# Kernel tuning notes

Hardware: AMD Instinct MI355X
Metric: run time of the kernel (lower is better)

The kernel has to match this reference:

```python
import jax, jax.numpy as jnp
import numpy as np

B = 16384
INPUT_DIM = 2048
HIDDEN = 1536
N_COMP = 256
N_LAYERS = 32
TOP_K = 4


def setup_inputs() -> dict:
    key = jax.random.key(0)
    ks = jax.random.split(key, 12)
    s_in = 1.0 / np.sqrt(INPUT_DIM)
    s_h = 1.0 / np.sqrt(HIDDEN)
    s_3 = 1.0 / np.sqrt(3)
    return {
        "x": jax.random.normal(ks[0], (B, INPUT_DIM), dtype=jnp.float32),
        "layer_idx": 3,
        "embed": jax.random.normal(ks[1], (N_LAYERS, INPUT_DIM), dtype=jnp.float32),
        "enc_w1": jax.random.uniform(ks[2], (INPUT_DIM, HIDDEN), jnp.float32, -s_in, s_in),
        "enc_b1": jax.random.uniform(ks[3], (HIDDEN,), jnp.float32, -s_in, s_in),
        "enc_w2": jax.random.uniform(ks[4], (HIDDEN, N_COMP), jnp.float32, -s_h, s_h),
        "enc_b2": jax.random.uniform(ks[5], (N_COMP,), jnp.float32, -s_h, s_h),
        "components": jax.random.normal(ks[6], (N_COMP, 3), dtype=jnp.float32),
        "dec_w1": jax.random.uniform(ks[7], (3, HIDDEN), jnp.float32, -s_3, s_3),
        "dec_b1": jax.random.uniform(ks[8], (HIDDEN,), jnp.float32, -s_3, s_3),
        "dec_w2": jax.random.uniform(ks[9], (HIDDEN, INPUT_DIM), jnp.float32, -s_h, s_h),
        "dec_b2": jax.random.uniform(ks[10], (INPUT_DIM,), jnp.float32, -s_h, s_h),
    }


def reference(x, layer_idx, embed, enc_w1, enc_b1, enc_w2, enc_b2,
              components, dec_w1, dec_b1, dec_w2, dec_b2):
    # x: (B, D). Add per-layer embedding row.
    x = x + embed[layer_idx]
    # Encoder MLP: Linear -> GELU (exact, erf-based like torch default) -> Linear
    h = jax.nn.gelu(x @ enc_w1 + enc_b1, approximate=False)
    logits = h @ enc_w2 + enc_b2                     # (B, C)
    # Top-k gated masked softmax: softmax over only the top_k logits per row.
    vals, idx = jax.lax.top_k(logits, TOP_K)         # (B, K), (B, K)
    w = jax.nn.softmax(vals, axis=-1)                # (B, K)
    # Sparse mix: equivalent to masked_fill(-inf) softmax @ components
    pts = jnp.einsum('bk,bkc->bc', w, components[idx])  # (B, 3)
    # Decoder MLP
    d = jax.nn.gelu(pts @ dec_w1 + dec_b1, approximate=False)
    decoded = d @ dec_w2 + dec_b2                    # (B, D)
    encoded = jnp.broadcast_to(components[None], (x.shape[0], N_COMP, 3))
    return encoded, decoded
```

## Files before the change

### kernel.cpp

```cpp
#include <hip/hip_runtime.h>


typedef float  f32x4  __attribute__((ext_vector_type(4)));
typedef short  short8 __attribute__((ext_vector_type(8)));
typedef int    i32x4  __attribute__((ext_vector_type(4)));

#define DEVINL __device__ __forceinline__

constexpr int  NB      = 16384;
constexpr int  IN_DIM  = 2048;
constexpr int  HID     = 1536;
constexpr int  NC      = 256;
constexpr long ENC_ELEMS = (long)NB * NC * 3;
constexpr float TAU  = 2e-5f;
constexpr float TAU1 = 1.5e-3f;
constexpr int  MAXR  = 64;
constexpr int  M2CAP = 2048;
constexpr int  NKT1 = IN_DIM / 32;
constexpr int  NKT2 = HID / 32;

constexpr float SCALE_X  = 3251.2f;
constexpr float SCALE_W1 = 1471325.0f;
constexpr float SCALE_H  = 4644.5714f;
constexpr float SCALE_W2 = 1274205.0f;
constexpr double INV_S1 = 1.0 / ((double)SCALE_X * (double)SCALE_W1);
constexpr double INV_S2 = 1.0 / ((double)SCALE_H * (double)SCALE_W2);
constexpr float C_DA     = 3.0f;
constexpr float SCALE_DA = 39.08f;
constexpr float SCALE_W2D = 4977.0f;
constexpr double INV_SD = 1.0 / ((double)SCALE_DA * (double)SCALE_W2D);

DEVINL unsigned short f2bf(float f) {
  unsigned int u = __builtin_bit_cast(unsigned int, f);
  u = u + 0x7fffu + ((u >> 16) & 1u);
  return (unsigned short)(u >> 16);
}
DEVINL float bf2f(unsigned short h) {
  unsigned int u = ((unsigned int)h) << 16;
  return __builtin_bit_cast(float, u);
}
DEVINL float gelu_f(float v) {
  return 0.5f * v * (1.0f + erff(v * 0.70710678118654752440f));
}
DEVINL void llds16(const void* g, void* l) {
  __builtin_amdgcn_global_load_lds(
      (const __attribute__((address_space(1))) void*)g,
      (__attribute__((address_space(3))) void*)l, 16, 0, 0);
}
DEVINL f32x4 mfma_bf16(short8 a, short8 b, f32x4 c) {
  return __builtin_amdgcn_mfma_f32_16x16x32_bf16(a, b, c, 0, 0, 0);
}
DEVINL i32x4 mfma_i8(i32x4 a, i32x4 b, i32x4 c) {
  return __builtin_amdgcn_mfma_i32_16x16x64_i8(a, b, c, 0, 0, 0);
}
DEVINL long packed_off(long tileIdx, int rowp, int kq, int e) {
  int slot = kq ^ ((rowp >> 1) & 3);
  return (tileIdx * 512 + rowp * 4 + slot) * 8 + e;
}
DEVINL int swz_idx(int rowp, int kq) {
  return (rowp * 4 + (kq ^ ((rowp >> 1) & 3))) * 8;
}
DEVINL long i8_off(long tile64, int rowp, int kin64) {
  return tile64 * 8192 + rowp * 64 + kin64;
}
DEVINL int quant16(float v, float scale) {
  int q = (int)lrintf(v * scale);
  if (q >  32512) q =  32512;
  if (q < -32512) q = -32512;
  return q;
}
DEVINL int quant8(float v, float scale) {
  int q = (int)lrintf(v * scale);
  if (q >  127) q =  127;
  if (q < -127) q = -127;
  return q;
}

__global__ __launch_bounds__(256) void transpose_split_kernel(
    const float* __restrict__ in, int K, int N, int nkt,
    unsigned short* __restrict__ outH, unsigned short* __restrict__ outL)
{
  __shared__ float t[32][33];
  int tx = threadIdx.x & 31, ty = threadIdx.x >> 5;
  int n0 = blockIdx.x * 32, k0 = blockIdx.y * 32;
#pragma unroll
  for (int i = 0; i < 4; ++i)
    t[ty + i * 8][tx] = in[(long)(k0 + ty + i * 8) * N + n0 + tx];
  __syncthreads();

  int n = n0 + tx;
  int ntile = n >> 7, rowp = n & 127;
  int Kt = k0 >> 5;
  int j = ty & 3;
  long off = packed_off((long)ntile * nkt + Kt, rowp, j, 0);
  if (ty < 4) {
    short8 hv;
#pragma unroll
    for (int e = 0; e < 8; ++e) hv[e] = (short)f2bf(t[j * 8 + e][tx]);
    *(short8*)(outH + off) = hv;
  } else if (outL) {
    short8 lv;
#pragma unroll
    for (int e = 0; e < 8; ++e) {
      float f = t[j * 8 + e][tx];
      lv[e] = (short)f2bf(f - bf2f(f2bf(f)));
    }
    *(short8*)(outL + off) = lv;
  }
}

__global__ __launch_bounds__(256) void transpose_quant_kernel(
    const float* __restrict__ in, int K, int N, int nkt64, float scale,
    char* __restrict__ outH, char* __restrict__ outL)
{
  __shared__ float t[32][33];
  int tx = threadIdx.x & 31, ty = threadIdx.x >> 5;
  int n0 = blockIdx.x * 32, k0 = blockIdx.y * 32;
#pragma unroll
  for (int i = 0; i < 4; ++i)
    t[ty + i * 8][tx] = in[(long)(k0 + ty + i * 8) * N + n0 + tx];
  __syncthreads();

  int n = n0 + tx;
  int j = ty & 3;
  int kb = k0 + j * 8;
  long off = i8_off((long)(n >> 7) * nkt64 + (kb >> 6), n & 127, kb & 63);
  union { char b[8]; long v; } u;
  if (ty < 4) {
#pragma unroll
    for (int e = 0; e < 8; ++e) {
      int q = quant16(t[j * 8 + e][tx], scale);
      int lo = (q << 24) >> 24;
      u.b[e] = (char)((q - lo) >> 8);
    }
    *(long*)(outH + off) = u.v;
  } else {
#pragma unroll
    for (int e = 0; e < 8; ++e) {
      int q = quant16(t[j * 8 + e][tx], scale);
      u.b[e] = (char)((q << 24) >> 24);
    }
    *(long*)(outL + off) = u.v;
  }
}

__global__ __launch_bounds__(256) void transpose_quant8_kernel(
    const float* __restrict__ in, int K, int N, int nkt64, float scale,
    char* __restrict__ outQ)
{
  __shared__ float t[32][33];
  int tx = threadIdx.x & 31, ty = threadIdx.x >> 5;
  int n0 = blockIdx.x * 32, k0 = blockIdx.y * 32;
#pragma unroll
  for (int i = 0; i < 4; ++i)
    t[ty + i * 8][tx] = in[(long)(k0 + ty + i * 8) * N + n0 + tx];
  __syncthreads();

  if (ty >= 4) return;
  int n = n0 + tx;
  int j = ty;
  int kb = k0 + j * 8;
  long off = i8_off((long)(n >> 7) * nkt64 + (kb >> 6), n & 127, kb & 63);
  union { char b[8]; long v; } u;
#pragma unroll
  for (int e = 0; e < 8; ++e)
    u.b[e] = (char)quant8(t[j * 8 + e][tx], scale);
  *(long*)(outQ + off) = u.v;
}

__global__ __launch_bounds__(256) void dec_bias_kernel(
    const float* __restrict__ W2d, const float* __restrict__ b2d,
    float* __restrict__ badj)
{
  int j = blockIdx.x * 256 + threadIdx.x;
  float s = 0.f;
  for (int k = 0; k < HID; ++k) s += W2d[(long)k * IN_DIM + j];
  badj[j] = b2d[j] + C_DA * s;
}

__global__ __launch_bounds__(256) void quant_x_kernel(
    const float* __restrict__ x, const float* __restrict__ embedMat,
    const int* __restrict__ liPtr, char* __restrict__ Xh, char* __restrict__ Xl,
    int* __restrict__ cnt, int* __restrict__ cnt2)
{
  if (blockIdx.x == 0 && threadIdx.x == 0) { *cnt = 0; *cnt2 = 0; }
  long g = (long)blockIdx.x * 256 + threadIdx.x;
  int row = (int)(g >> 7);
  int k0 = ((int)(g & 127)) * 16;
  int li = liPtr[0];
  const float* xr = x + (long)row * IN_DIM + k0;
  const float* er = embedMat + (long)li * IN_DIM + k0;
  union { char b[16]; i32x4 v; } hu, lu;
#pragma unroll
  for (int c = 0; c < 4; ++c) {
    f32x4 a = *(const f32x4*)(xr + c * 4);
    f32x4 e = *(const f32x4*)(er + c * 4);
#pragma unroll
    for (int jj = 0; jj < 4; ++jj) {
      int q = quant16(a[jj] + e[jj], SCALE_X);
      int lo = (q << 24) >> 24;
      hu.b[c * 4 + jj] = (char)((q - lo) >> 8);
      lu.b[c * 4 + jj] = (char)lo;
    }
  }
  long off = i8_off((long)(row >> 7) * (IN_DIM / 64) + (k0 >> 6), row & 127, k0 & 63);
  *(i32x4*)(Xh + off) = hu.v;
  *(i32x4*)(Xl + off) = lu.v;
}

template<int OUT, int PRODUCTS>
__global__ __launch_bounds__(256, 2) void gemm_i8_kernel(
    const char* __restrict__ Ah, const char* __restrict__ Al,
    const char* __restrict__ Bh, const char* __restrict__ Bl,
    int nkt64, const float* __restrict__ bias, double invScale,
    float* __restrict__ Cf, long ldc,
    char* __restrict__ Qh, char* __restrict__ Ql, int nktOut64, float outScale,
    int nbn)
{
  __shared__ alignas(16) char sAh[8192];
  __shared__ alignas(16) char sAl[PRODUCTS == 3 ? 8192 : 16];
  __shared__ alignas(16) char sBh[8192];
  __shared__ alignas(16) char sBl[PRODUCTS == 3 ? 8192 : 16];
  __shared__ float sBias[128];

  int tid = threadIdx.x;
  int nwg = gridDim.x, q = nwg >> 3, b0 = blockIdx.x;
  int sw = (b0 & 7) * q + (b0 >> 3);
  int bm = sw / nbn, bn = sw % nbn;

  if (tid < 128) sBias[tid] = bias[bn * 128 + tid];

  int wid = tid >> 6, lane = tid & 63;
  int wm = wid >> 1, wn = wid & 1;
  int l15 = lane & 15, kq = lane >> 4;

  i32x4 accH[4][4] = {};
  i32x4 accM[4][4] = {};

  for (int kt = 0; kt < nkt64; ++kt) {
    __syncthreads();
    {
      const char* g0 = Ah + ((long)(bm * nkt64 + kt)) * 8192 + tid * 16;
      llds16(g0, sAh + tid * 16); llds16(g0 + 4096, sAh + 4096 + tid * 16);
      const char* g2 = Bh + ((long)(bn * nkt64 + kt)) * 8192 + tid * 16;
      llds16(g2, sBh + tid * 16); llds16(g2 + 4096, sBh + 4096 + tid * 16);
      if constexpr (PRODUCTS == 3) {
        const char* g1 = Al + ((long)(bm * nkt64 + kt)) * 8192 + tid * 16;
        llds16(g1, sAl + tid * 16); llds16(g1 + 4096, sAl + 4096 + tid * 16);
        const char* g3 = Bl + ((long)(bn * nkt64 + kt)) * 8192 + tid * 16;
        llds16(g3, sBl + tid * 16); llds16(g3 + 4096, sBl + 4096 + tid * 16);
      }
    }
    __syncthreads();

    i32x4 bhf[4], blf[4];
#pragma unroll
    for (int n = 0; n < 4; ++n) {
      int off = (wn * 64 + n * 16 + l15) * 64 + kq * 16;
      bhf[n] = *(const i32x4*)&sBh[off];
      if constexpr (PRODUCTS == 3) blf[n] = *(const i32x4*)&sBl[off];
    }
#pragma unroll
    for (int m = 0; m < 4; ++m) {
      int off = (wm * 64 + m * 16 + l15) * 64 + kq * 16;
      i32x4 ahf = *(const i32x4*)&sAh[off];
      i32x4 alf;
      if constexpr (PRODUCTS == 3) alf = *(const i32x4*)&sAl[off];
#pragma unroll
      for (int n = 0; n < 4; ++n) {
        accH[m][n] = mfma_i8(ahf, bhf[n], accH[m][n]);
        if constexpr (PRODUCTS == 3) {
          accM[m][n] = mfma_i8(alf, bhf[n], accM[m][n]);
          accM[m][n] = mfma_i8(ahf, blf[n], accM[m][n]);
        }
      }
    }
  }

#pragma unroll
  for (int m = 0; m < 4; ++m) {
#pragma unroll
    for (int n = 0; n < 4; ++n) {
      int  gcol = bn * 128 + wn * 64 + n * 16 + l15;
      float bb  = sBias[wn * 64 + n * 16 + l15];
#pragma unroll
      for (int r = 0; r < 4; ++r) {
        long grow = (long)bm * 128 + wm * 64 + m * 16 + kq * 4 + r;
        double dv;
        if constexpr (PRODUCTS == 3)
          dv = (double)accH[m][n][r] * 65536.0 + (double)accM[m][n][r] * 256.0;
        else
          dv = (double)accH[m][n][r];
        float v = (float)(dv * invScale) + bb;
        if constexpr (OUT == 0) {
          Cf[grow * ldc + gcol] = v;
        } else {
          v = gelu_f(v);
          int qq = quant16(v, outScale);
          int lo = (qq << 24) >> 24;
          long off = i8_off((long)(grow >> 7) * nktOut64 + (gcol >> 6),
                            (int)(grow & 127), gcol & 63);
          Qh[off] = (char)((qq - lo) >> 8);
          Ql[off] = (char)lo;
        }
      }
    }
  }
}

template<bool SPLIT, int OUT_MODE, bool GELU, int KU>
__global__ __launch_bounds__(256) void gemm2_kernel(
    const unsigned short* __restrict__ Ah, const unsigned short* __restrict__ Al,
    const unsigned short* __restrict__ Bh, const unsigned short* __restrict__ Bl,
    int nkt, const float* __restrict__ bias, float* __restrict__ Cf,
    unsigned short* __restrict__ Ch, unsigned short* __restrict__ Cl,
    long ldc, int nktOut, int nbn, const int* __restrict__ mrows, int mcap)
{
  __shared__ alignas(16) unsigned short sAh[4096 * KU];
  __shared__ alignas(16) unsigned short sAl[SPLIT ? 4096 * KU : 8];
  __shared__ alignas(16) unsigned short sBh[4096 * KU];
  __shared__ alignas(16) unsigned short sBl[SPLIT ? 4096 * KU : 8];
  __shared__ float sBias[128];

  int tid = threadIdx.x;
  int nwg = gridDim.x, q = nwg >> 3, b0 = blockIdx.x;
  int sw = (b0 & 7) * q + (b0 >> 3);
  int bm = sw / nbn, bn = sw % nbn;

  if (mrows) {
    int v = *mrows; if (v > mcap) v = mcap;
    if (bm * 128 >= v) return;
  }

  if (tid < 128) sBias[tid] = bias[bn * 128 + tid];

  int wid = tid >> 6, lane = tid & 63;
  int wm = wid >> 1, wn = wid & 1;
  int l15 = lane & 15, kq = lane >> 4;

  f32x4 acc[4][4] = {};

  for (int kt = 0; kt < nkt; kt += KU) {
    __syncthreads();
#pragma unroll
    for (int u = 0; u < KU; ++u) {
      {
        const char* gA = (const char*)Ah + ((long)(bm * nkt + kt + u)) * 8192 + tid * 16;
        llds16(gA,        (char*)sAh + u * 8192 + tid * 16);
        llds16(gA + 4096, (char*)sAh + u * 8192 + 4096 + tid * 16);
      }
      if constexpr (SPLIT) {
        const char* gA = (const char*)Al + ((long)(bm * nkt + kt + u)) * 8192 + tid * 16;
        llds16(gA,        (char*)sAl + u * 8192 + tid * 16);
        llds16(gA + 4096, (char*)sAl + u * 8192 + 4096 + tid * 16);
      }
      {
        const char* gB = (const char*)Bh + ((long)(bn * nkt + kt + u)) * 8192 + tid * 16;
        llds16(gB,        (char*)sBh + u * 8192 + tid * 16);
        llds16(gB + 4096, (char*)sBh + u * 8192 + 4096 + tid * 16);
      }
      if constexpr (SPLIT) {
        const char* gB = (const char*)Bl + ((long)(bn * nkt + kt + u)) * 8192 + tid * 16;
        llds16(gB,        (char*)sBl + u * 8192 + tid * 16);
        llds16(gB + 4096, (char*)sBl + u * 8192 + 4096 + tid * 16);
      }
    }
    __syncthreads();

#pragma unroll
    for (int u = 0; u < KU; ++u) {
      short8 bh[4], bl[4];
#pragma unroll
      for (int n = 0; n < 4; ++n) {
        int idx = u * 4096 + swz_idx(wn * 64 + n * 16 + l15, kq);
        bh[n] = *(const short8*)&sBh[idx];
        if constexpr (SPLIT) bl[n] = *(const short8*)&sBl[idx];
      }
#pragma unroll
      for (int m = 0; m < 4; ++m) {
        int idx = u * 4096 + swz_idx(wm * 64 + m * 16 + l15, kq);
        short8 ah = *(const short8*)&sAh[idx];
        short8 al;
        if constexpr (SPLIT) al = *(const short8*)&sAl[idx];
#pragma unroll
        for (int n = 0; n < 4; ++n) {
          acc[m][n] = mfma_bf16(ah, bh[n], acc[m][n]);
          if constexpr (SPLIT) {
            acc[m][n] = mfma_bf16(al, bh[n], acc[m][n]);
            acc[m][n] = mfma_bf16(ah, bl[n], acc[m][n]);
          }
        }
      }
    }
  }

#pragma unroll
  for (int m = 0; m < 4; ++m) {
#pragma unroll
    for (int n = 0; n < 4; ++n) {
      int  gcol = bn * 128 + wn * 64 + n * 16 + l15;
      float bb  = sBias[wn * 64 + n * 16 + l15];
#pragma unroll
      for (int r = 0; r < 4; ++r) {
        long grow = (long)bm * 128 + wm * 64 + m * 16 + kq * 4 + r;
        float v = acc[m][n][r] + bb;
        if constexpr (GELU) v = gelu_f(v);
        if constexpr (OUT_MODE == 0) {
          Cf[grow * ldc + gcol] = v;
        } else {
          int Mt = (int)(grow >> 7), rowpo = (int)(grow & 127);
          int Kt = gcol >> 5, kqo = (gcol >> 3) & 3, e = gcol & 7;
          long off = packed_off((long)Mt * nktOut + Kt, rowpo, kqo, e);
          unsigned short hb = f2bf(v);
          Ch[off] = hb;
          Cl[off] = f2bf(v - bf2f(hb));
        }
      }
    }
  }
}

__global__ __launch_bounds__(256) void topk_screen_kernel(
    const float* __restrict__ logits, const float* __restrict__ comp,
    float* __restrict__ pts, float* __restrict__ encOut,
    int* __restrict__ cnt2, int* __restrict__ list2,
    int* __restrict__ rescueCnt, int* __restrict__ rescueList)
{
  int wid = threadIdx.x >> 6, lane = threadIdx.x & 63;
  long row = (long)blockIdx.x * 4 + wid;
  f32x4 v4 = *(const f32x4*)(logits + row * NC + lane * 4);
  float a[4] = {v4[0], v4[1], v4[2], v4[3]};

  float tv[5]; int ti[5];
#pragma unroll
  for (int t = 0; t < 5; ++t) {
    float lv = a[0]; int li = lane * 4;
#pragma unroll
    for (int i = 1; i < 4; ++i)
      if (a[i] > lv) { lv = a[i]; li = lane * 4 + i; }
#pragma unroll
    for (int off = 32; off >= 1; off >>= 1) {
      float ov = __shfl_xor(lv, off);
      int   oi = __shfl_xor(li, off);
      if (ov > lv || (ov == lv && oi < li)) { lv = ov; li = oi; }
    }
    tv[t] = lv; ti[t] = li;
    if (t < 4 && (li >> 2) == lane) a[li & 3] = -INFINITY;
  }

  bool flag = (tv[3] - tv[4]) < TAU1;
  if (!flag) {
    float m = tv[0], w[4], s = 0.f;
#pragma unroll
    for (int t = 0; t < 4; ++t) { w[t] = expf(tv[t] - m); s += w[t]; }
    float inv = 1.0f / s;
    if (lane < 3) {
      float p = 0.f;
#pragma unroll
      for (int t = 0; t < 4; ++t) p += w[t] * inv * comp[ti[t] * 3 + lane];
      pts[row * 3 + lane] = p;
    }
  } else if (lane == 0) {
    int pos = atomicAdd(cnt2, 1);
    if (pos < M2CAP) list2[pos] = (int)row;
    else { int rp = atomicAdd(rescueCnt, 1); rescueList[rp] = (int)row; }
  }

  const f32x4* cv = (const f32x4*)comp;
  f32x4* ov = (f32x4*)encOut + (long)blockIdx.x * 768;
  for (int j = threadIdx.x; j < 768; j += 256)
    ov[j] = cv[j % 192];
}

__global__ __launch_bounds__(256) void gather_kernel(
    const float* __restrict__ x, const float* __restrict__ embedMat,
    const int* __restrict__ liPtr, const int* __restrict__ cnt2,
    const int* __restrict__ list2,
    unsigned short* __restrict__ A2h, unsigned short* __restrict__ A2l)
{
  int i = blockIdx.x;
  int c2 = *cnt2; if (c2 > M2CAP) c2 = M2CAP;
  if (i >= c2) return;
  int row = list2[i];
  int li = liPtr[0];
  int t = threadIdx.x;
  int k0 = t * 8;
  const float* xr = x + (long)row * IN_DIM + k0;
  const float* er = embedMat + (long)li * IN_DIM + k0;
  short8 hv, lv;
#pragma unroll
  for (int c = 0; c < 2; ++c) {
    f32x4 a = *(const f32x4*)(xr + c * 4);
    f32x4 e = *(const f32x4*)(er + c * 4);
#pragma unroll
    for (int jj = 0; jj < 4; ++jj) {
      float f = a[jj] + e[jj];
      unsigned short hb = f2bf(f);
      hv[c * 4 + jj] = (short)hb;
      lv[c * 4 + jj] = (short)f2bf(f - bf2f(hb));
    }
  }
  long off = packed_off((long)(i >> 7) * NKT1 + (k0 >> 5), i & 127, (k0 >> 3) & 3, 0);
  *(short8*)(A2h + off) = hv;
  *(short8*)(A2l + off) = lv;
}

__global__ __launch_bounds__(256) void topk_final_kernel(
    const float* __restrict__ logits2, const float* __restrict__ comp,
    const int* __restrict__ cnt2, const int* __restrict__ list2,
    float* __restrict__ pts, int* __restrict__ rescueCnt, int* __restrict__ rescueList)
{
  int wid = threadIdx.x >> 6, lane = threadIdx.x & 63;
  int slot = blockIdx.x * 4 + wid;
  int c2 = *cnt2; if (c2 > M2CAP) c2 = M2CAP;
  if (slot >= c2) return;
  int row = list2[slot];
  f32x4 v4 = *(const f32x4*)(logits2 + (long)slot * NC + lane * 4);
  float a[4] = {v4[0], v4[1], v4[2], v4[3]};

  float tv[5]; int ti[5];
#pragma unroll
  for (int t = 0; t < 5; ++t) {
    float lv = a[0]; int li = lane * 4;
#pragma unroll
    for (int i = 1; i < 4; ++i)
      if (a[i] > lv) { lv = a[i]; li = lane * 4 + i; }
#pragma unroll
    for (int off = 32; off >= 1; off >>= 1) {
      float ov = __shfl_xor(lv, off);
      int   oi = __shfl_xor(li, off);
      if (ov > lv || (ov == lv && oi < li)) { lv = ov; li = oi; }
    }
    tv[t] = lv; ti[t] = li;
    if (t < 4 && (li >> 2) == lane) a[li & 3] = -INFINITY;
  }

  float m = tv[0], w[4], s = 0.f;
#pragma unroll
  for (int t = 0; t < 4; ++t) { w[t] = expf(tv[t] - m); s += w[t]; }
  float inv = 1.0f / s;
  if (lane < 3) {
    float p = 0.f;
#pragma unroll
    for (int t = 0; t < 4; ++t) p += w[t] * inv * comp[ti[t] * 3 + lane];
    pts[(long)row * 3 + lane] = p;
  }
  if (lane == 0 && (tv[3] - tv[4]) < TAU) {
    int pos = atomicAdd(rescueCnt, 1);
    rescueList[pos] = row;
  }
}

__global__ __launch_bounds__(256) void rescue_h1_kernel(
    const float* __restrict__ x, const float* __restrict__ embedMat,
    const int* __restrict__ liPtr, const float* __restrict__ W1,
    const int* __restrict__ cnt, const int* __restrict__ list,
    double* __restrict__ partial)
{
  int b = blockIdx.x;
  int s = b / 24, rem = b % 24;
  int cc = rem >> 2, kp = rem & 3;
  int n = *cnt;
  if (s >= n || s >= MAXR) return;
  int row = list[s];
  __shared__ double xd[512];
  int tid = threadIdx.x;
  int li = liPtr[0];
  int k0 = kp * 512;
  for (int j = tid; j < 512; j += 256)
    xd[j] = (double)x[(long)row * IN_DIM + k0 + j]
          + (double)embedMat[(long)li * IN_DIM + k0 + j];
  __syncthreads();
  int c = cc * 256 + tid;
  const float* wp = W1 + (long)k0 * HID + c;
  double s0 = 0, s1 = 0, s2 = 0, s3 = 0;
  for (int k = 0; k < 512; k += 4) {
    s0 += xd[k]     * (double)wp[(long)k * HID];
    s1 += xd[k + 1] * (double)wp[(long)(k + 1) * HID];
    s2 += xd[k + 2] * (double)wp[(long)(k + 2) * HID];
    s3 += xd[k + 3] * (double)wp[(long)(k + 3) * HID];
  }
  partial[((long)(s * 6 + cc) * 4 + kp) * 256 + tid] = (s0 + s1) + (s2 + s3);
}

__global__ __launch_bounds__(256) void rescue_h2_kernel(
    const float* __restrict__ b1, const int* __restrict__ cnt,
    const double* __restrict__ partial, double* __restrict__ hbuf)
{
  int b = blockIdx.x;
  int s = b / 6, cc = b % 6;
  int n = *cnt;
  if (s >= n || s >= MAXR) return;
  int tid = threadIdx.x;
  long base = ((long)(s * 6 + cc) * 4) * 256 + tid;
  double v = (double)b1[cc * 256 + tid]
           + ((partial[base] + partial[base + 256])
            + (partial[base + 512] + partial[base + 768]));
  hbuf[(long)s * HID + cc * 256 + tid]
      = 0.5 * v * (1.0 + erf(v * 0.70710678118654752440));
}

__global__ __launch_bounds__(256) void rescue_logits_kernel(
    const float* __restrict__ W2, const float* __restrict__ b2,
    const float* __restrict__ comp, const int* __restrict__ cnt,
    const int* __restrict__ list, const double* __restrict__ hbuf,
    float* __restrict__ pts)
{
  int s = blockIdx.x;
  int n = *cnt;
  if (s >= n || s >= MAXR) return;
  __shared__ double hd[HID];
  __shared__ double ld[NC];
  int tid = threadIdx.x;
  for (int j = tid; j < HID; j += 256) hd[j] = hbuf[(long)s * HID + j];
  __syncthreads();
  {
    const float* wp = W2 + tid;
    double a0 = 0, a1 = 0, a2 = 0, a3 = 0;
    for (int k = 0; k < HID; k += 4) {
      a0 += hd[k]     * (double)wp[(long)k * NC];
      a1 += hd[k + 1] * (double)wp[(long)(k + 1) * NC];
      a2 += hd[k + 2] * (double)wp[(long)(k + 2) * NC];
      a3 += hd[k + 3] * (double)wp[(long)(k + 3) * NC];
    }
    ld[tid] = (double)b2[tid] + ((a0 + a1) + (a2 + a3));
  }
  __syncthreads();
  if (tid == 0) {
    int row = list[s];
    int idx[4]; double val[4];
    unsigned long long mask[4] = {0, 0, 0, 0};
    for (int t = 0; t < 4; ++t) {
      double bv = -1e300; int bi = 0;
      for (int j = 0; j < NC; ++j) {
        if ((mask[j >> 6] >> (j & 63)) & 1ull) continue;
        if (ld[j] > bv) { bv = ld[j]; bi = j; }
      }
      idx[t] = bi; val[t] = bv; mask[bi >> 6] |= 1ull << (bi & 63);
    }
    double m = val[0], w[4], sum = 0;
    for (int t = 0; t < 4; ++t) { w[t] = exp(val[t] - m); sum += w[t]; }
    for (int c = 0; c < 3; ++c) {
      double p = 0;
      for (int t = 0; t < 4; ++t) p += (w[t] / sum) * (double)comp[idx[t] * 3 + c];
      pts[(long)row * 3 + c] = (float)p;
    }
  }
}

__global__ __launch_bounds__(256) void rescue_slow_kernel(
    const float* __restrict__ x, const float* __restrict__ embedMat,
    const int* __restrict__ liPtr, const float* __restrict__ W1,
    const float* __restrict__ b1, const float* __restrict__ W2,
    const float* __restrict__ b2, const float* __restrict__ comp,
    float* __restrict__ pts, const int* __restrict__ cnt, const int* __restrict__ list)
{
  __shared__ double xd[IN_DIM];
  __shared__ double hd[HID];
  __shared__ double ld[NC];
  int tid = threadIdx.x;
  int li = liPtr[0];
  int n = *cnt;
  for (int it = MAXR + blockIdx.x; it < n; it += gridDim.x) {
    int row = list[it];
    const float* xr = x + (long)row * IN_DIM;
    const float* er = embedMat + (long)li * IN_DIM;
    for (int j = tid; j < IN_DIM; j += 256)
      xd[j] = (double)xr[j] + (double)er[j];
    __syncthreads();
    for (int c = tid; c < HID; c += 256) {
      double s0 = 0, s1 = 0, s2 = 0, s3 = 0;
      const float* wp = W1 + c;
      for (int k = 0; k < IN_DIM; k += 4) {
        s0 += xd[k]     * (double)wp[(long)k * HID];
        s1 += xd[k + 1] * (double)wp[(long)(k + 1) * HID];
        s2 += xd[k + 2] * (double)wp[(long)(k + 2) * HID];
        s3 += xd[k + 3] * (double)wp[(long)(k + 3) * HID];
      }
      double s = (double)b1[c] + ((s0 + s1) + (s2 + s3));
      hd[c] = 0.5 * s * (1.0 + erf(s * 0.70710678118654752440));
    }
    __syncthreads();
    {
      int c = tid;
      double s0 = 0, s1 = 0, s2 = 0, s3 = 0;
      const float* wp = W2 + c;
      for (int k = 0; k < HID; k += 4) {
        s0 += hd[k]     * (double)wp[(long)k * NC];
        s1 += hd[k + 1] * (double)wp[(long)(k + 1) * NC];
        s2 += hd[k + 2] * (double)wp[(long)(k + 2) * NC];
        s3 += hd[k + 3] * (double)wp[(long)(k + 3) * NC];
      }
      ld[c] = (double)b2[c] + ((s0 + s1) + (s2 + s3));
    }
    __syncthreads();
    if (tid == 0) {
      int idx[4]; double val[4];
      unsigned long long mask[4] = {0, 0, 0, 0};
      for (int t = 0; t < 4; ++t) {
        double bv = -1e300; int bi = 0;
        for (int j = 0; j < NC; ++j) {
          if ((mask[j >> 6] >> (j & 63)) & 1ull) continue;
          if (ld[j] > bv) { bv = ld[j]; bi = j; }
        }
        idx[t] = bi; val[t] = bv; mask[bi >> 6] |= 1ull << (bi & 63);
      }
      double m = val[0], w[4], s = 0;
      for (int t = 0; t < 4; ++t) { w[t] = exp(val[t] - m); s += w[t]; }
      for (int c = 0; c < 3; ++c) {
        double p = 0;
        for (int t = 0; t < 4; ++t) p += (w[t] / s) * (double)comp[idx[t] * 3 + c];
        pts[(long)row * 3 + c] = (float)p;
      }
    }
    __syncthreads();
  }
}

__global__ __launch_bounds__(256) void dec_a_kernel(
    const float* __restrict__ pts, const float* __restrict__ W1d,
    const float* __restrict__ b1d, char* __restrict__ dq)
{
  for (long u = blockIdx.x; u < (long)NB * 6; u += gridDim.x) {
    int  j = (int)(u % 6) * 256 + threadIdx.x;
    long b = u / 6;
    const float* p = pts + b * 3;
    float s = fmaf(p[0], W1d[j], fmaf(p[1], W1d[HID + j], fmaf(p[2], W1d[2 * HID + j], b1d[j])));
    float d = gelu_f(s);
    int q = quant8(d - C_DA, SCALE_DA);
    int Mt = (int)(b >> 7), rowp = (int)(b & 127);
    dq[i8_off((long)Mt * (HID / 64) + (j >> 6), rowp, j & 63)] = (char)q;
  }
}

extern "C" void kernel_launch(void* const* d_in, const int* in_sizes, int n_in,
                              void* d_out, int out_size, void* d_ws, size_t ws_size,
                              hipStream_t stream) {
  const float* x     = (const float*)d_in[0];
  const int*   liPtr = (const int*)  d_in[1];
  const float* embed = (const float*)d_in[2];
  const float* W1    = (const float*)d_in[3];
  const float* b1    = (const float*)d_in[4];
  const float* W2    = (const float*)d_in[5];
  const float* b2    = (const float*)d_in[6];
  const float* comp  = (const float*)d_in[7];
  const float* W1d   = (const float*)d_in[8];
  const float* b1d   = (const float*)d_in[9];
  const float* W2d   = (const float*)d_in[10];
  const float* b2d   = (const float*)d_in[11];
  float* out = (float*)d_out;

  char* w = (char*)d_ws;
  unsigned short* W1hT = (unsigned short*)(w);
  unsigned short* W1lT = (unsigned short*)(w + 6291456);
  unsigned short* W2hT = (unsigned short*)(w + 12582912);
  unsigned short* W2lT = (unsigned short*)(w + 13369344);
  char*  W2dq = w + 14155776;
  float* badj = (float*)(w + 17301504);
  char* W1qh = w + 20447232;
  char* W1ql = w + 23592960;
  char* W2qh = w + 26738688;
  char* W2ql = w + 27131904;
  char* Xqh = w + 27525120;
  char* Xql = w + 61079552;
  char* Hqh = w + 94633984;
  char* Hql = w + 119799808;
  float* logits = (float*)(w + 144965632);
  unsigned short* A2h = (unsigned short*)(w + 161742848);
  unsigned short* A2l = (unsigned short*)(w + 178520064);
  unsigned short* H2h = (unsigned short*)(w + 195297280);
  unsigned short* H2l = (unsigned short*)(w + 207880192);
  float* logits2 = (float*)(w + 220463104);
  char*  dq = w + 27525120;
  float* pts   = (float*)(w + 224657408);
  int*   cnt   = (int*)  (w + 224854016);
  int*   cnt2  = (int*)  (w + 224854272);
  int*   list  = (int*)  (w + 224854528);
  int*   list2 = (int*)  (w + 224920064);
  double* partial = (double*)(w + 224936448);
  double* hbuf    = (double*)(w + 228082176);

  transpose_split_kernel<<<dim3(HID / 32, IN_DIM / 32), 256, 0, stream>>>(W1, IN_DIM, HID, NKT1, W1hT, W1lT);
  transpose_split_kernel<<<dim3(NC / 32, HID / 32),     256, 0, stream>>>(W2, HID, NC, NKT2, W2hT, W2lT);
  transpose_quant_kernel<<<dim3(HID / 32, IN_DIM / 32), 256, 0, stream>>>(W1, IN_DIM, HID, IN_DIM / 64, SCALE_W1, W1qh, W1ql);
  transpose_quant_kernel<<<dim3(NC / 32, HID / 32),     256, 0, stream>>>(W2, HID, NC, HID / 64, SCALE_W2, W2qh, W2ql);
  transpose_quant8_kernel<<<dim3(IN_DIM / 32, HID / 32), 256, 0, stream>>>(W2d, HID, IN_DIM, HID / 64, SCALE_W2D, W2dq);
  dec_bias_kernel<<<IN_DIM / 256, 256, 0, stream>>>(W2d, b2d, badj);

  quant_x_kernel<<<NB * 128 / 256, 256, 0, stream>>>(x, embed, liPtr, Xqh, Xql, cnt, cnt2);
  gemm_i8_kernel<1, 3><<<(NB / 128) * (HID / 128), 256, 0, stream>>>(
      Xqh, Xql, W1qh, W1ql, IN_DIM / 64, b1, INV_S1,
      nullptr, 0, Hqh, Hql, HID / 64, SCALE_H, HID / 128);
  gemm_i8_kernel<0, 3><<<(NB / 128) * (NC / 128), 256, 0, stream>>>(
      Hqh, Hql, W2qh, W2ql, HID / 64, b2, INV_S2,
      logits, NC, nullptr, nullptr, 0, 0.f, NC / 128);

  topk_screen_kernel<<<NB / 4, 256, 0, stream>>>(logits, comp, pts, out, cnt2, list2, cnt, list);

  gather_kernel<<<M2CAP, 256, 0, stream>>>(x, embed, liPtr, cnt2, list2, A2h, A2l);
  gemm2_kernel<true, 2, true, 4><<<(M2CAP / 128) * (HID / 128), 256, 0, stream>>>(
      A2h, A2l, W1hT, W1lT, NKT1, b1, nullptr, H2h, H2l, 0, NKT2, HID / 128, cnt2, M2CAP);
  gemm2_kernel<true, 0, false, 4><<<(M2CAP / 128) * (NC / 128), 256, 0, stream>>>(
      H2h, H2l, W2hT, W2lT, NKT2, b2, logits2, nullptr, nullptr, NC, 0, NC / 128, cnt2, M2CAP);
  topk_final_kernel<<<M2CAP / 4, 256, 0, stream>>>(logits2, comp, cnt2, list2, pts, cnt, list);

  rescue_h1_kernel<<<MAXR * 24, 256, 0, stream>>>(x, embed, liPtr, W1, cnt, list, partial);
  rescue_h2_kernel<<<MAXR * 6,  256, 0, stream>>>(b1, cnt, partial, hbuf);
  rescue_logits_kernel<<<MAXR,  256, 0, stream>>>(W2, b2, comp, cnt, list, hbuf, pts);
  rescue_slow_kernel<<<64, 256, 0, stream>>>(x, embed, liPtr, W1, b1, W2, b2, comp, pts, cnt, list);

  dec_a_kernel<<<3072, 256, 0, stream>>>(pts, W1d, b1d, dq);
  gemm_i8_kernel<0, 1><<<(NB / 128) * (IN_DIM / 128), 256, 0, stream>>>(
      dq, nullptr, W2dq, nullptr, HID / 64, badj, INV_SD,
      out + ENC_ELEMS, IN_DIM, nullptr, nullptr, 0, 0.f, IN_DIM / 128);
}
```

Before: 726.6 us.

## Fuse weight/input prep kernels into one launch and merge rescue_h2 into logits

Seven small prep kernels (bf16 split transposes, int8 quant transposes of W1/W2/W2d, the decoder bias sum and the x quantization) become one block-indexed mega kernel. W1 and W2 are now read once for both the bf16 split and the int8 quant outputs. The rescue_h2 stage is folded into rescue_logits, so the hbuf round trip and one launch are gone. The costs are a heavier mega kernel with mixed block roles and load imbalance, since the dec_bias blocks run a long serial loop.

```diff
diff --git a/kernel.cpp b/kernel.cpp
--- a/kernel.cpp
+++ b/kernel.cpp
@@ -76,136 +76,135 @@
   return q;
 }
 
-__global__ __launch_bounds__(256) void transpose_split_kernel(
-    const float* __restrict__ in, int K, int N, int nkt,
-    unsigned short* __restrict__ outH, unsigned short* __restrict__ outL)
-{
+__global__ __launch_bounds__(256) void mega_prep_kernel(
+    const float* __restrict__ W1, const float* __restrict__ W2,
+    const float* __restrict__ W2d, const float* __restrict__ b2d,
+    const float* __restrict__ x, const float* __restrict__ embedMat,
+    const int* __restrict__ liPtr,
+    unsigned short* __restrict__ W1hT, unsigned short* __restrict__ W1lT,
+    unsigned short* __restrict__ W2hT, unsigned short* __restrict__ W2lT,
+    char* __restrict__ W1qh, char* __restrict__ W1ql,
+    char* __restrict__ W2qh, char* __restrict__ W2ql,
+    char* __restrict__ W2dq, float* __restrict__ badj,
+    char* __restrict__ Xh, char* __restrict__ Xl,
+    int* __restrict__ cnt, int* __restrict__ cnt2)
+{
+  constexpr int E0 = 3072;
+  constexpr int E1 = E0 + 384;
+  constexpr int E2 = E1 + 3072;
+  constexpr int E3 = E2 + 8;
+  constexpr int E4 = E3 + 8192;
+  int b = blockIdx.x;
+  int tid = threadIdx.x;
   __shared__ float t[32][33];
-  int tx = threadIdx.x & 31, ty = threadIdx.x >> 5;
-  int n0 = blockIdx.x * 32, k0 = blockIdx.y * 32;
-#pragma unroll
-  for (int i = 0; i < 4; ++i)
-    t[ty + i * 8][tx] = in[(long)(k0 + ty + i * 8) * N + n0 + tx];
-  __syncthreads();
-
-  int n = n0 + tx;
-  int ntile = n >> 7, rowp = n & 127;
-  int Kt = k0 >> 5;
-  int j = ty & 3;
-  long off = packed_off((long)ntile * nkt + Kt, rowp, j, 0);
-  if (ty < 4) {
-    short8 hv;
-#pragma unroll
-    for (int e = 0; e < 8; ++e) hv[e] = (short)f2bf(t[j * 8 + e][tx]);
-    *(short8*)(outH + off) = hv;
-  } else if (outL) {
-    short8 lv;
-#pragma unroll
-    for (int e = 0; e < 8; ++e) {
-      float f = t[j * 8 + e][tx];
-      lv[e] = (short)f2bf(f - bf2f(f2bf(f)));
-    }
-    *(short8*)(outL + off) = lv;
-  }
-}
-
-__global__ __launch_bounds__(256) void transpose_quant_kernel(
-    const float* __restrict__ in, int K, int N, int nkt64, float scale,
-    char* __restrict__ outH, char* __restrict__ outL)
-{
-  __shared__ float t[32][33];
-  int tx = threadIdx.x & 31, ty = threadIdx.x >> 5;
-  int n0 = blockIdx.x * 32, k0 = blockIdx.y * 32;
-#pragma unroll
-  for (int i = 0; i < 4; ++i)
-    t[ty + i * 8][tx] = in[(long)(k0 + ty + i * 8) * N + n0 + tx];
-  __syncthreads();
-
-  int n = n0 + tx;
-  int j = ty & 3;
-  int kb = k0 + j * 8;
-  long off = i8_off((long)(n >> 7) * nkt64 + (kb >> 6), n & 127, kb & 63);
-  union { char b[8]; long v; } u;
-  if (ty < 4) {
-#pragma unroll
-    for (int e = 0; e < 8; ++e) {
-      int q = quant16(t[j * 8 + e][tx], scale);
-      int lo = (q << 24) >> 24;
-      u.b[e] = (char)((q - lo) >> 8);
-    }
-    *(long*)(outH + off) = u.v;
+
+  if (b < E1) {
+    const float* in; int N, nktB, nkt64; float qscale;
+    unsigned short *oH, *oL; char *qH, *qL;
+    int bx, by;
+    if (b < E0) { in = W1;  N = HID; nktB = NKT1; nkt64 = IN_DIM / 64;
+                  qscale = SCALE_W1; oH = W1hT; oL = W1lT; qH = W1qh; qL = W1ql;
+                  bx = b % 48; by = b / 48; }
+    else        { int bb = b - E0;
+                  in = W2;  N = NC;  nktB = NKT2; nkt64 = HID / 64;
+                  qscale = SCALE_W2; oH = W2hT; oL = W2lT; qH = W2qh; qL = W2ql;
+                  bx = bb % 8; by = bb / 8; }
+    int tx = tid & 31, ty = tid >> 5;
+    int n0 = bx * 32, k0 = by * 32;
+#pragma unroll
+    for (int i = 0; i < 4; ++i)
+      t[ty + i * 8][tx] = in[(long)(k0 + ty + i * 8) * N + n0 + tx];
+    __syncthreads();
+    int n = n0 + tx;
+    int j = ty & 3;
+    {
+      long off = packed_off((long)(n >> 7) * nktB + (k0 >> 5), n & 127, j, 0);
+      if (ty < 4) {
+        short8 hv;
+#pragma unroll
+        for (int e = 0; e < 8; ++e) hv[e] = (short)f2bf(t[j * 8 + e][tx]);
+        *(short8*)(oH + off) = hv;
+      } else {
+        short8 lv;
+#pragma unroll
+        for (int e = 0; e < 8; ++e) {
+          float f = t[j * 8 + e][tx];
+          lv[e] = (short)f2bf(f - bf2f(f2bf(f)));
+        }
+        *(short8*)(oL + off) = lv;
+      }
+    }
+    {
+      int kb = k0 + j * 8;
+      long off = i8_off((long)(n >> 7) * nkt64 + (kb >> 6), n & 127, kb & 63);
+      union { char b[8]; long v; } u;
+      if (ty < 4) {
+#pragma unroll
+        for (int e = 0; e < 8; ++e) {
+          int q = quant16(t[j * 8 + e][tx], qscale);
+          int lo = (q << 24) >> 24;
+          u.b[e] = (char)((q - lo) >> 8);
+        }
+        *(long*)(qH + off) = u.v;
+      } else {
+#pragma unroll
+        for (int e = 0; e < 8; ++e) {
+          int q = quant16(t[j * 8 + e][tx], qscale);
+          u.b[e] = (char)((q << 24) >> 24);
+        }
+        *(long*)(qL + off) = u.v;
+      }
+    }
+  } else if (b < E2) {
+    int bb = b - E1;
+    int bx = bb % 64, by = bb / 64;
+    int tx = tid & 31, ty = tid >> 5;
+    int n0 = bx * 32, k0 = by * 32;
+#pragma unroll
+    for (int i = 0; i < 4; ++i)
+      t[ty + i * 8][tx] = W2d[(long)(k0 + ty + i * 8) * IN_DIM + n0 + tx];
+    __syncthreads();
+    if (ty < 4) {
+      int n = n0 + tx;
+      int kb = k0 + ty * 8;
+      long off = i8_off((long)(n >> 7) * (HID / 64) + (kb >> 6), n & 127, kb & 63);
+      union { char b[8]; long v; } u;
+#pragma unroll
+      for (int e = 0; e < 8; ++e)
+        u.b[e] = (char)quant8(t[ty * 8 + e][tx], SCALE_W2D);
+      *(long*)(W2dq + off) = u.v;
+    }
+  } else if (b < E3) {
+    int j = (b - E2) * 256 + tid;
+    float s = 0.f;
+    for (int k = 0; k < HID; ++k) s += W2d[(long)k * IN_DIM + j];
+    badj[j] = b2d[j] + C_DA * s;
+  } else if (b < E4) {
+    long g = (long)(b - E3) * 256 + tid;
+    int row = (int)(g >> 7);
+    int k0 = ((int)(g & 127)) * 16;
+    int li = liPtr[0];
+    const float* xr = x + (long)row * IN_DIM + k0;
+    const float* er = embedMat + (long)li * IN_DIM + k0;
+    union { char b[16]; i32x4 v; } hu, lu;
+#pragma unroll
+    for (int c = 0; c < 4; ++c) {
+      f32x4 a = *(const f32x4*)(xr + c * 4);
+      f32x4 e = *(const f32x4*)(er + c * 4);
+#pragma unroll
+      for (int jj = 0; jj < 4; ++jj) {
+        int q = quant16(a[jj] + e[jj], SCALE_X);
+        int lo = (q << 24) >> 24;
+        hu.b[c * 4 + jj] = (char)((q - lo) >> 8);
+        lu.b[c * 4 + jj] = (char)lo;
+      }
+    }
+    long off = i8_off((long)(row >> 7) * (IN_DIM / 64) + (k0 >> 6), row & 127, k0 & 63);
+    *(i32x4*)(Xh + off) = hu.v;
+    *(i32x4*)(Xl + off) = lu.v;
   } else {
-#pragma unroll
-    for (int e = 0; e < 8; ++e) {
-      int q = quant16(t[j * 8 + e][tx], scale);
-      u.b[e] = (char)((q << 24) >> 24);
-    }
-    *(long*)(outL + off) = u.v;
-  }
-}
-
-__global__ __launch_bounds__(256) void transpose_quant8_kernel(
-    const float* __restrict__ in, int K, int N, int nkt64, float scale,
-    char* __restrict__ outQ)
-{
-  __shared__ float t[32][33];
-  int tx = threadIdx.x & 31, ty = threadIdx.x >> 5;
-  int n0 = blockIdx.x * 32, k0 = blockIdx.y * 32;
-#pragma unroll
-  for (int i = 0; i < 4; ++i)
-    t[ty + i * 8][tx] = in[(long)(k0 + ty + i * 8) * N + n0 + tx];
-  __syncthreads();
-
-  if (ty >= 4) return;
-  int n = n0 + tx;
-  int j = ty;
-  int kb = k0 + j * 8;
-  long off = i8_off((long)(n >> 7) * nkt64 + (kb >> 6), n & 127, kb & 63);
-  union { char b[8]; long v; } u;
-#pragma unroll
-  for (int e = 0; e < 8; ++e)
-    u.b[e] = (char)quant8(t[j * 8 + e][tx], scale);
-  *(long*)(outQ + off) = u.v;
-}
-
-__global__ __launch_bounds__(256) void dec_bias_kernel(
-    const float* __restrict__ W2d, const float* __restrict__ b2d,
-    float* __restrict__ badj)
-{
-  int j = blockIdx.x * 256 + threadIdx.x;
-  float s = 0.f;
-  for (int k = 0; k < HID; ++k) s += W2d[(long)k * IN_DIM + j];
-  badj[j] = b2d[j] + C_DA * s;
-}
-
-__global__ __launch_bounds__(256) void quant_x_kernel(
-    const float* __restrict__ x, const float* __restrict__ embedMat,
-    const int* __restrict__ liPtr, char* __restrict__ Xh, char* __restrict__ Xl,
-    int* __restrict__ cnt, int* __restrict__ cnt2)
-{
-  if (blockIdx.x == 0 && threadIdx.x == 0) { *cnt = 0; *cnt2 = 0; }
-  long g = (long)blockIdx.x * 256 + threadIdx.x;
-  int row = (int)(g >> 7);
-  int k0 = ((int)(g & 127)) * 16;
-  int li = liPtr[0];
-  const float* xr = x + (long)row * IN_DIM + k0;
-  const float* er = embedMat + (long)li * IN_DIM + k0;
-  union { char b[16]; i32x4 v; } hu, lu;
-#pragma unroll
-  for (int c = 0; c < 4; ++c) {
-    f32x4 a = *(const f32x4*)(xr + c * 4);
-    f32x4 e = *(const f32x4*)(er + c * 4);
-#pragma unroll
-    for (int jj = 0; jj < 4; ++jj) {
-      int q = quant16(a[jj] + e[jj], SCALE_X);
-      int lo = (q << 24) >> 24;
-      hu.b[c * 4 + jj] = (char)((q - lo) >> 8);
-      lu.b[c * 4 + jj] = (char)lo;
-    }
-  }
-  long off = i8_off((long)(row >> 7) * (IN_DIM / 64) + (k0 >> 6), row & 127, k0 & 63);
-  *(i32x4*)(Xh + off) = hu.v;
-  *(i32x4*)(Xl + off) = lu.v;
+    if (tid == 0) { *cnt = 0; *cnt2 = 0; }
+  }
 }
 
 template<int OUT, int PRODUCTS>
@@ -583,28 +582,11 @@
   partial[((long)(s * 6 + cc) * 4 + kp) * 256 + tid] = (s0 + s1) + (s2 + s3);
 }
 
-__global__ __launch_bounds__(256) void rescue_h2_kernel(
-    const float* __restrict__ b1, const int* __restrict__ cnt,
-    const double* __restrict__ partial, double* __restrict__ hbuf)
-{
-  int b = blockIdx.x;
-  int s = b / 6, cc = b % 6;
-  int n = *cnt;
-  if (s >= n || s >= MAXR) return;
-  int tid = threadIdx.x;
-  long base = ((long)(s * 6 + cc) * 4) * 256 + tid;
-  double v = (double)b1[cc * 256 + tid]
-           + ((partial[base] + partial[base + 256])
-            + (partial[base + 512] + partial[base + 768]));
-  hbuf[(long)s * HID + cc * 256 + tid]
-      = 0.5 * v * (1.0 + erf(v * 0.70710678118654752440));
-}
-
 __global__ __launch_bounds__(256) void rescue_logits_kernel(
-    const float* __restrict__ W2, const float* __restrict__ b2,
-    const float* __restrict__ comp, const int* __restrict__ cnt,
-    const int* __restrict__ list, const double* __restrict__ hbuf,
-    float* __restrict__ pts)
+    const float* __restrict__ b1, const float* __restrict__ W2,
+    const float* __restrict__ b2, const float* __restrict__ comp,
+    const int* __restrict__ cnt, const int* __restrict__ list,
+    const double* __restrict__ partial, float* __restrict__ pts)
 {
   int s = blockIdx.x;
   int n = *cnt;
@@ -612,7 +594,13 @@
   __shared__ double hd[HID];
   __shared__ double ld[NC];
   int tid = threadIdx.x;
-  for (int j = tid; j < HID; j += 256) hd[j] = hbuf[(long)s * HID + j];
+  for (int cc = 0; cc < 6; ++cc) {
+    long base = ((long)(s * 6 + cc) * 4) * 256 + tid;
+    double v = (double)b1[cc * 256 + tid]
+             + ((partial[base] + partial[base + 256])
+              + (partial[base + 512] + partial[base + 768]));
+    hd[cc * 256 + tid] = 0.5 * v * (1.0 + erf(v * 0.70710678118654752440));
+  }
   __syncthreads();
   {
     const float* wp = W2 + tid;
@@ -778,16 +766,12 @@
   int*   list  = (int*)  (w + 224854528);
   int*   list2 = (int*)  (w + 224920064);
   double* partial = (double*)(w + 224936448);
-  double* hbuf    = (double*)(w + 228082176);
-
-  transpose_split_kernel<<<dim3(HID / 32, IN_DIM / 32), 256, 0, stream>>>(W1, IN_DIM, HID, NKT1, W1hT, W1lT);
-  transpose_split_kernel<<<dim3(NC / 32, HID / 32),     256, 0, stream>>>(W2, HID, NC, NKT2, W2hT, W2lT);
-  transpose_quant_kernel<<<dim3(HID / 32, IN_DIM / 32), 256, 0, stream>>>(W1, IN_DIM, HID, IN_DIM / 64, SCALE_W1, W1qh, W1ql);
-  transpose_quant_kernel<<<dim3(NC / 32, HID / 32),     256, 0, stream>>>(W2, HID, NC, HID / 64, SCALE_W2, W2qh, W2ql);
-  transpose_quant8_kernel<<<dim3(IN_DIM / 32, HID / 32), 256, 0, stream>>>(W2d, HID, IN_DIM, HID / 64, SCALE_W2D, W2dq);
-  dec_bias_kernel<<<IN_DIM / 256, 256, 0, stream>>>(W2d, b2d, badj);
-
-  quant_x_kernel<<<NB * 128 / 256, 256, 0, stream>>>(x, embed, liPtr, Xqh, Xql, cnt, cnt2);
+
+  mega_prep_kernel<<<14729, 256, 0, stream>>>(
+      W1, W2, W2d, b2d, x, embed, liPtr,
+      W1hT, W1lT, W2hT, W2lT, W1qh, W1ql, W2qh, W2ql,
+      W2dq, badj, Xqh, Xql, cnt, cnt2);
+
   gemm_i8_kernel<1, 3><<<(NB / 128) * (HID / 128), 256, 0, stream>>>(
       Xqh, Xql, W1qh, W1ql, IN_DIM / 64, b1, INV_S1,
       nullptr, 0, Hqh, Hql, HID / 64, SCALE_H, HID / 128);
@@ -805,8 +789,7 @@
   topk_final_kernel<<<M2CAP / 4, 256, 0, stream>>>(logits2, comp, cnt2, list2, pts, cnt, list);
 
   rescue_h1_kernel<<<MAXR * 24, 256, 0, stream>>>(x, embed, liPtr, W1, cnt, list, partial);
-  rescue_h2_kernel<<<MAXR * 6,  256, 0, stream>>>(b1, cnt, partial, hbuf);
-  rescue_logits_kernel<<<MAXR,  256, 0, stream>>>(W2, b2, comp, cnt, list, hbuf, pts);
+  rescue_logits_kernel<<<MAXR, 256, 0, stream>>>(b1, W2, b2, comp, cnt, list, partial, pts);
   rescue_slow_kernel<<<64, 256, 0, stream>>>(x, embed, liPtr, W1, b1, W2, b2, comp, pts, cnt, list);
 
   dec_a_kernel<<<3072, 256, 0, stream>>>(pts, W1d, b1d, dq);
```

After: 712.6 us. About the same (-1.9%).
